# Kernel optimization log

Measured on AMD Instinct MI355X. Metric: run time of the kernel, lower is better.

## Reference

```python
import jax, jax.numpy as jnp
import numpy as np

B, S, D, H = 4, 2048, 768, 12
HD = D // H  # head_dim = 64


def setup_inputs() -> dict:
    key = jax.random.key(0)
    k1, k2, k3, k4, k5 = jax.random.split(key, 5)
    scale = 0.02
    return {
        "x": jax.random.normal(k1, (B, S, D), dtype=jnp.float32),
        "w_qkv": jax.random.normal(k2, (D, 3 * D), dtype=jnp.float32) * scale,
        "b_qkv": jax.random.normal(k3, (3 * D,), dtype=jnp.float32) * scale,
        "w_proj": jax.random.normal(k4, (D, D), dtype=jnp.float32) * scale,
        "b_proj": jax.random.normal(k5, (D,), dtype=jnp.float32) * scale,
    }


def reference(x, w_qkv, b_qkv, w_proj, b_proj):
    b, s, d = x.shape
    # fused qkv projection: (b, s, 3d) -> (3, b, h, s, hd)
    qkv = x @ w_qkv + b_qkv
    qkv = qkv.reshape(b, s, 3, H, HD).transpose(2, 0, 3, 1, 4)
    q, k, v = qkv[0], qkv[1], qkv[2]
    # scaled dot-product attention with explicit (b, h, s, s) scores
    scores = jnp.einsum("bhqd,bhkd->bhqk", q, k) / jnp.sqrt(jnp.float32(HD))
    attn = jax.nn.softmax(scores, axis=-1)
    out = jnp.einsum("bhqk,bhkd->bhqd", attn, v)
    out = out.transpose(0, 2, 1, 3).reshape(b, s, d)  # concat heads
    return out @ w_proj + b_proj
```

## Files before the change

kernel.cpp:

```cpp
#include <hip/hip_runtime.h>
#include <hip/hip_bf16.h>
#include <stdint.h>


typedef __attribute__((ext_vector_type(8))) short bf16x8;
typedef __attribute__((ext_vector_type(4))) short bf16x4;
typedef __attribute__((ext_vector_type(4))) float f32x4;
typedef __attribute__((ext_vector_type(4))) unsigned short u16x4;

__device__ __forceinline__ unsigned short f2bf(float x) {
  union { float f; uint32_t u; } v; v.f = x;
  uint32_t r = v.u + 0x7FFF + ((v.u >> 16) & 1);
  return (unsigned short)(r >> 16);
}

__device__ __forceinline__ uint32_t cvtpk_bf16(float lo, float hi) {
  uint32_t r;
  asm("v_cvt_pk_bf16_f32 %0, %1, %2" : "=v"(r) : "v"(lo), "v"(hi));
  return r;
}

__device__ __forceinline__ void gload_lds16(const void* g, void* l) {
  __builtin_amdgcn_global_load_lds(
      (const __attribute__((address_space(1))) void*)g,
      (__attribute__((address_space(3))) void*)l, 16, 0, 0);
}

__global__ void cast_x_kernel(const float* __restrict__ x,
                              unsigned short* __restrict__ xb, int n) {
  int idx = (blockIdx.x * blockDim.x + threadIdx.x) * 4;
  if (idx < n) {
    f32x4 v = *(const f32x4*)(x + idx);
    u16x4 o;
    o[0] = f2bf(v[0]); o[1] = f2bf(v[1]); o[2] = f2bf(v[2]); o[3] = f2bf(v[3]);
    *(u16x4*)(xb + idx) = o;
  }
}

__global__ void transpose_cast_kernel(const float* __restrict__ W,
                                      unsigned short* __restrict__ Wt,
                                      int K, int N) {
  __shared__ float tile[64][65];
  int k0 = blockIdx.y * 64, n0 = blockIdx.x * 64;
  int t = threadIdx.x;
#pragma unroll
  for (int i = 0; i < 16; i++) {
    int idx = i * 256 + t; int r = idx >> 6, c = idx & 63;
    tile[r][c] = W[(size_t)(k0 + r) * N + n0 + c];
  }
  __syncthreads();
#pragma unroll
  for (int i = 0; i < 16; i++) {
    int idx = i * 256 + t; int r = idx >> 6, c = idx & 63;
    Wt[(size_t)(n0 + r) * K + k0 + c] = f2bf(tile[c][r]);
  }
}

template <int EPI>
__global__ __launch_bounds__(256, 2) void gemm_kernel(
    const unsigned short* __restrict__ A,
    const unsigned short* __restrict__ Bt,
    const float* __restrict__ bias,
    void* __restrict__ out0,
    unsigned short* __restrict__ Kb,
    unsigned short* __restrict__ Vt,
    int M, int N, int K) {
  __shared__ unsigned short As[128 * 64];
  __shared__ unsigned short Bs[128 * 64];
  const int tid = threadIdx.x;
  const int wave = tid >> 6, lane = tid & 63;
  const int wm = wave >> 1, wn = wave & 1;
  const int m0 = blockIdx.y * 128, n0 = blockIdx.x * 128;
  const int g = lane >> 4, c16 = lane & 15;
  f32x4 acc[4][4] = {};

  for (int k0 = 0; k0 < K; k0 += 64) {
    int rb = wave * 32;
#pragma unroll
    for (int j = 0; j < 4; j++) {
      int r = rb + j * 8 + (lane >> 3);
      int ca = (lane & 7) ^ (r & 7);
      gload_lds16(A + (size_t)(m0 + r) * K + k0 + ca * 8, As + (rb + j * 8) * 64);
      gload_lds16(Bt + (size_t)(n0 + r) * K + k0 + ca * 8, Bs + (rb + j * 8) * 64);
    }
    __syncthreads();
#pragma unroll
    for (int ks = 0; ks < 2; ks++) {
      bf16x8 af[4], bfr[4];
#pragma unroll
      for (int mi = 0; mi < 4; mi++) {
        int row = wm * 64 + mi * 16 + c16;
        int ch = (ks * 4 + g) ^ (row & 7);
        af[mi] = *(const bf16x8*)(As + row * 64 + ch * 8);
      }
#pragma unroll
      for (int nj = 0; nj < 4; nj++) {
        int row = wn * 64 + nj * 16 + c16;
        int ch = (ks * 4 + g) ^ (row & 7);
        bfr[nj] = *(const bf16x8*)(Bs + row * 64 + ch * 8);
      }
#pragma unroll
      for (int mi = 0; mi < 4; mi++)
#pragma unroll
        for (int nj = 0; nj < 4; nj++)
          acc[mi][nj] = __builtin_amdgcn_mfma_f32_16x16x32_bf16(
              af[mi], bfr[nj], acc[mi][nj], 0, 0, 0);
    }
    __syncthreads();
  }

  if (EPI == 0) {
    const float QSC = 0.125f * 1.44269504088896f;
    unsigned short* Qb = (unsigned short*)out0;
#pragma unroll
    for (int nj = 0; nj < 4; nj++) {
      int n = n0 + wn * 64 + nj * 16 + c16;
      int t = n / 768, rr = n % 768;
      int h = rr >> 6, d = rr & 63;
      float bv = bias[n];
#pragma unroll
      for (int mi = 0; mi < 4; mi++) {
        int mrow = m0 + wm * 64 + mi * 16 + g * 4;
        int b = mrow >> 11, s = mrow & 2047;
        if (t == 0) {
          size_t base = ((size_t)(b * 12 + h) * 2048 + s) * 64 + d;
#pragma unroll
          for (int rg = 0; rg < 4; rg++)
            Qb[base + (size_t)rg * 64] = f2bf((acc[mi][nj][rg] + bv) * QSC);
        } else if (t == 1) {
          size_t base = ((size_t)(b * 12 + h) * 2048 + s) * 64 + d;
#pragma unroll
          for (int rg = 0; rg < 4; rg++)
            Kb[base + (size_t)rg * 64] = f2bf(acc[mi][nj][rg] + bv);
        } else {
          u16x4 p;
          p[0] = f2bf(acc[mi][nj][0] + bv);
          p[1] = f2bf(acc[mi][nj][1] + bv);
          p[2] = f2bf(acc[mi][nj][2] + bv);
          p[3] = f2bf(acc[mi][nj][3] + bv);
          *(u16x4*)(Vt + ((size_t)(b * 12 + h) * 64 + d) * 2048 + s) = p;
        }
      }
    }
  } else {
    float* outp = (float*)out0;
#pragma unroll
    for (int nj = 0; nj < 4; nj++) {
      int n = n0 + wn * 64 + nj * 16 + c16;
      float bv = bias[n];
#pragma unroll
      for (int mi = 0; mi < 4; mi++) {
        int mrow = m0 + wm * 64 + mi * 16 + g * 4;
#pragma unroll
        for (int rg = 0; rg < 4; rg++)
          outp[(size_t)(mrow + rg) * N + n] = acc[mi][nj][rg] + bv;
      }
    }
  }
}

__global__ __launch_bounds__(256, 4) void attn_kernel(
    const unsigned short* __restrict__ Qb,
    const unsigned short* __restrict__ Kb,
    const unsigned short* __restrict__ Vt,
    unsigned short* __restrict__ Ao) {
  __shared__ unsigned short Ks[64 * 64];
  __shared__ unsigned short Vs[64 * 64];
  const int id = blockIdx.x;
  const int xcd = id & 7, slot = id >> 3;
  const int bh = xcd * 6 + (slot % 6);
  const int q0 = (slot / 6) * 128;
  const int tid = threadIdx.x;
  const int wave = tid >> 6, lane = tid & 63;
  const int g = lane >> 4, c16 = lane & 15;
  const int rw = c16 & 7;
  const int rb = wave * 16;

  bf16x8 qf[2][2];
  {
    const unsigned short* qp =
        Qb + ((size_t)bh * 2048 + q0 + wave * 32 + c16) * 64;
#pragma unroll
    for (int qa = 0; qa < 2; qa++) {
      qf[qa][0] = *(const bf16x8*)(qp + qa * 1024 + g * 8);
      qf[qa][1] = *(const bf16x8*)(qp + qa * 1024 + 32 + g * 8);
    }
  }
  f32x4 acc_o[2][4] = {};
  float l_run[2] = {0.f, 0.f};
  const int alane = (lane & 48) + g * 4;

  for (int kt = 0; kt < 32; kt++) {
#pragma unroll
    for (int j = 0; j < 2; j++) {
      int r = rb + j * 8 + (lane >> 3);
      int ca = (lane & 7) ^ (r & 7);
      gload_lds16(Kb + ((size_t)bh * 2048 + kt * 64 + r) * 64 + ca * 8,
                  Ks + (rb + j * 8) * 64);
      gload_lds16(Vt + ((size_t)bh * 64 + r) * 2048 + kt * 64 + ca * 8,
                  Vs + (rb + j * 8) * 64);
    }
    __syncthreads();

    f32x4 sacc[2][4] = {};
#pragma unroll
    for (int ks = 0; ks < 2; ks++) {
#pragma unroll
      for (int nf = 0; nf < 4; nf++) {
        int row = nf * 16 + c16;
        int ch = (ks * 4 + g) ^ (row & 7);
        bf16x8 kf = *(const bf16x8*)(Ks + row * 64 + ch * 8);
        sacc[0][nf] =
            __builtin_amdgcn_mfma_f32_16x16x32_bf16(kf, qf[0][ks], sacc[0][nf], 0, 0, 0);
        sacc[1][nf] =
            __builtin_amdgcn_mfma_f32_16x16x32_bf16(kf, qf[1][ks], sacc[1][nf], 0, 0, 0);
      }
    }

#pragma unroll
    for (int qa = 0; qa < 2; qa++) {
      float rs = 0.f;
#pragma unroll
      for (int nf = 0; nf < 4; nf++) {
        sacc[qa][nf][0] = __builtin_amdgcn_exp2f(sacc[qa][nf][0]);
        sacc[qa][nf][1] = __builtin_amdgcn_exp2f(sacc[qa][nf][1]);
        sacc[qa][nf][2] = __builtin_amdgcn_exp2f(sacc[qa][nf][2]);
        sacc[qa][nf][3] = __builtin_amdgcn_exp2f(sacc[qa][nf][3]);
        rs += (sacc[qa][nf][0] + sacc[qa][nf][1]) +
              (sacc[qa][nf][2] + sacc[qa][nf][3]);
      }
      rs += __shfl_xor(rs, 16);
      rs += __shfl_xor(rs, 32);
      l_run[qa] += rs;
    }

#pragma unroll
    for (int ks = 0; ks < 2; ks++) {
      union { uint32_t w[4]; bf16x8 v8; } pa0, pa1;
      pa0.w[0] = cvtpk_bf16(sacc[0][2 * ks][0], sacc[0][2 * ks][1]);
      pa0.w[1] = cvtpk_bf16(sacc[0][2 * ks][2], sacc[0][2 * ks][3]);
      pa0.w[2] = cvtpk_bf16(sacc[0][2 * ks + 1][0], sacc[0][2 * ks + 1][1]);
      pa0.w[3] = cvtpk_bf16(sacc[0][2 * ks + 1][2], sacc[0][2 * ks + 1][3]);
      pa1.w[0] = cvtpk_bf16(sacc[1][2 * ks][0], sacc[1][2 * ks][1]);
      pa1.w[1] = cvtpk_bf16(sacc[1][2 * ks][2], sacc[1][2 * ks][3]);
      pa1.w[2] = cvtpk_bf16(sacc[1][2 * ks + 1][0], sacc[1][2 * ks + 1][1]);
      pa1.w[3] = cvtpk_bf16(sacc[1][2 * ks + 1][2], sacc[1][2 * ks + 1][3]);
      const int c_lo = ks * 4 + (g >> 1);
      const int hwo = (g & 1) * 4;
#pragma unroll
      for (int nf = 0; nf < 4; nf++) {
        int row = nf * 16 + c16;
        union { struct { bf16x4 lo, hi; } h; bf16x8 v8; } vf;
        vf.h.lo = *(const bf16x4*)(&Vs[row * 64 + (c_lo ^ rw) * 8 + hwo]);
        vf.h.hi = *(const bf16x4*)(&Vs[row * 64 + ((c_lo + 2) ^ rw) * 8 + hwo]);
        acc_o[0][nf] =
            __builtin_amdgcn_mfma_f32_16x16x32_bf16(pa0.v8, vf.v8, acc_o[0][nf], 0, 0, 0);
        acc_o[1][nf] =
            __builtin_amdgcn_mfma_f32_16x16x32_bf16(pa1.v8, vf.v8, acc_o[1][nf], 0, 0, 0);
      }
    }
    __syncthreads();
  }

  const int b = bh / 12, h = bh % 12;
#pragma unroll
  for (int qa = 0; qa < 2; qa++) {
    float l_q[4];
#pragma unroll
    for (int rg = 0; rg < 4; rg++)
      l_q[rg] = __shfl(l_run[qa], alane + rg);
#pragma unroll
    for (int nf = 0; nf < 4; nf++) {
#pragma unroll
      for (int rg = 0; rg < 4; rg++) {
        float v = acc_o[qa][nf][rg] / l_q[rg];
        int srow = q0 + wave * 32 + qa * 16 + g * 4 + rg;
        Ao[((size_t)(b * 2048 + srow)) * 768 + h * 64 + nf * 16 + c16] = f2bf(v);
      }
    }
  }
}

extern "C" void kernel_launch(void* const* d_in, const int* in_sizes, int n_in,
                              void* d_out, int out_size, void* d_ws, size_t ws_size,
                              hipStream_t stream) {
  const float* x      = (const float*)d_in[0];
  const float* w_qkv  = (const float*)d_in[1];
  const float* b_qkv  = (const float*)d_in[2];
  const float* w_proj = (const float*)d_in[3];
  const float* b_proj = (const float*)d_in[4];

  unsigned short* xb  = (unsigned short*)d_ws;
  unsigned short* wqt = xb + 6291456;
  unsigned short* wpt = wqt + 1769472;
  unsigned short* Qb  = wpt + 589824;
  unsigned short* Kb  = Qb + 6291456;
  unsigned short* Vt  = Kb + 6291456;
  unsigned short* Ao  = Vt + 6291456;

  cast_x_kernel<<<6144, 256, 0, stream>>>(x, xb, 6291456);
  transpose_cast_kernel<<<dim3(36, 12), 256, 0, stream>>>(w_qkv, wqt, 768, 2304);
  transpose_cast_kernel<<<dim3(12, 12), 256, 0, stream>>>(w_proj, wpt, 768, 768);

  gemm_kernel<0><<<dim3(18, 64), 256, 0, stream>>>(
      xb, wqt, b_qkv, (void*)Qb, Kb, Vt, 8192, 2304, 768);

  attn_kernel<<<768, 256, 0, stream>>>(Qb, Kb, Vt, Ao);

  gemm_kernel<1><<<dim3(6, 64), 256, 0, stream>>>(
      Ao, wpt, b_proj, d_out, nullptr, nullptr, 8192, 768, 768);
}
```

Baseline: 152.1 us.

## Permute V layout for single 16-byte LDS reads and defer row-sum reduction

```diff
diff --git a/kernel.cpp b/kernel.cpp
--- a/kernel.cpp
+++ b/kernel.cpp
@@ -4,7 +4,6 @@
 
 
 typedef __attribute__((ext_vector_type(8))) short bf16x8;
-typedef __attribute__((ext_vector_type(4))) short bf16x4;
 typedef __attribute__((ext_vector_type(4))) float f32x4;
 typedef __attribute__((ext_vector_type(4))) unsigned short u16x4;
 
@@ -133,12 +132,13 @@
           for (int rg = 0; rg < 4; rg++)
             Kb[base + (size_t)rg * 64] = f2bf(acc[mi][nj][rg] + bv);
         } else {
+          int sp = (s & ~31) + (((s >> 2) & 3) << 3) + (((s >> 4) & 1) << 2);
           u16x4 p;
           p[0] = f2bf(acc[mi][nj][0] + bv);
           p[1] = f2bf(acc[mi][nj][1] + bv);
           p[2] = f2bf(acc[mi][nj][2] + bv);
           p[3] = f2bf(acc[mi][nj][3] + bv);
-          *(u16x4*)(Vt + ((size_t)(b * 12 + h) * 64 + d) * 2048 + s) = p;
+          *(u16x4*)(Vt + ((size_t)(b * 12 + h) * 64 + d) * 2048 + sp) = p;
         }
       }
     }
@@ -176,6 +176,11 @@
   const int rw = c16 & 7;
   const int rb = wave * 16;
 
+  const int sr = rb + (lane >> 3);
+  const int sca = (lane & 7) ^ (sr & 7);
+  const unsigned short* kp = Kb + ((size_t)bh * 2048 + sr) * 64 + sca * 8;
+  const unsigned short* vp = Vt + ((size_t)bh * 64 + sr) * 2048 + sca * 8;
+
   bf16x8 qf[2][2];
   {
     const unsigned short* qp =
@@ -191,15 +196,12 @@
   const int alane = (lane & 48) + g * 4;
 
   for (int kt = 0; kt < 32; kt++) {
-#pragma unroll
-    for (int j = 0; j < 2; j++) {
-      int r = rb + j * 8 + (lane >> 3);
-      int ca = (lane & 7) ^ (r & 7);
-      gload_lds16(Kb + ((size_t)bh * 2048 + kt * 64 + r) * 64 + ca * 8,
-                  Ks + (rb + j * 8) * 64);
-      gload_lds16(Vt + ((size_t)bh * 64 + r) * 2048 + kt * 64 + ca * 8,
-                  Vs + (rb + j * 8) * 64);
-    }
+    gload_lds16(kp, Ks + rb * 64);
+    gload_lds16(kp + 8 * 64, Ks + (rb + 8) * 64);
+    gload_lds16(vp, Vs + rb * 64);
+    gload_lds16(vp + 8 * 2048, Vs + (rb + 8) * 64);
+    kp += 64 * 64;
+    vp += 64;
     __syncthreads();
 
     f32x4 sacc[2][4] = {};
@@ -229,8 +231,6 @@
         rs += (sacc[qa][nf][0] + sacc[qa][nf][1]) +
               (sacc[qa][nf][2] + sacc[qa][nf][3]);
       }
-      rs += __shfl_xor(rs, 16);
-      rs += __shfl_xor(rs, 32);
       l_run[qa] += rs;
     }
 
@@ -245,18 +245,15 @@
       pa1.w[1] = cvtpk_bf16(sacc[1][2 * ks][2], sacc[1][2 * ks][3]);
       pa1.w[2] = cvtpk_bf16(sacc[1][2 * ks + 1][0], sacc[1][2 * ks + 1][1]);
       pa1.w[3] = cvtpk_bf16(sacc[1][2 * ks + 1][2], sacc[1][2 * ks + 1][3]);
-      const int c_lo = ks * 4 + (g >> 1);
-      const int hwo = (g & 1) * 4;
 #pragma unroll
       for (int nf = 0; nf < 4; nf++) {
         int row = nf * 16 + c16;
-        union { struct { bf16x4 lo, hi; } h; bf16x8 v8; } vf;
-        vf.h.lo = *(const bf16x4*)(&Vs[row * 64 + (c_lo ^ rw) * 8 + hwo]);
-        vf.h.hi = *(const bf16x4*)(&Vs[row * 64 + ((c_lo + 2) ^ rw) * 8 + hwo]);
+        int ch = (ks * 4 + g) ^ rw;
+        bf16x8 vf = *(const bf16x8*)(&Vs[row * 64 + ch * 8]);
         acc_o[0][nf] =
-            __builtin_amdgcn_mfma_f32_16x16x32_bf16(pa0.v8, vf.v8, acc_o[0][nf], 0, 0, 0);
+            __builtin_amdgcn_mfma_f32_16x16x32_bf16(pa0.v8, vf, acc_o[0][nf], 0, 0, 0);
         acc_o[1][nf] =
-            __builtin_amdgcn_mfma_f32_16x16x32_bf16(pa1.v8, vf.v8, acc_o[1][nf], 0, 0, 0);
+            __builtin_amdgcn_mfma_f32_16x16x32_bf16(pa1.v8, vf, acc_o[1][nf], 0, 0, 0);
       }
     }
     __syncthreads();
@@ -265,10 +262,13 @@
   const int b = bh / 12, h = bh % 12;
 #pragma unroll
   for (int qa = 0; qa < 2; qa++) {
+    float t = l_run[qa];
+    t += __shfl_xor(t, 16);
+    t += __shfl_xor(t, 32);
     float l_q[4];
 #pragma unroll
     for (int rg = 0; rg < 4; rg++)
-      l_q[rg] = __shfl(l_run[qa], alane + rg);
+      l_q[rg] = __shfl(t, alane + rg);
 #pragma unroll
     for (int nf = 0; nf < 4; nf++) {
 #pragma unroll
```

Result: faster. 143.7 us (-5.5%).
